# Kernel optimization log

Measured on AMD Instinct MI355X. Metric: run time of the kernel, lower is better.

The kernel has to match this reference:

```python
import jax, jax.numpy as jnp
import numpy as np

SAME_RANGE = 0.2  # depth tolerance for averaging splats at the same target pixel


def setup_inputs() -> dict:
    key = jax.random.key(0)
    k1, k2, k3 = jax.random.split(key, 3)
    B, C, H, W = 8, 3, 512, 1024
    obj = jax.random.normal(k1, (B, C, H, W), dtype=jnp.float32)
    flow = jax.random.normal(k2, (B, 2, H, W), dtype=jnp.float32)
    depth = jax.random.uniform(k3, (B, 1, H, W), dtype=jnp.float32)
    return {"obj": obj, "flow": flow, "depth": depth}


def reference(obj, flow, depth):
    # Forward-warping splat with per-target-pixel depth (z-buffer) test.
    # For each source pixel: warp by flow, round to nearest target pixel,
    # keep/average contributions whose depth is within same_range of the
    # minimum depth landing on that target pixel.
    B, C, H, W = obj.shape
    # p0: meshgrid with indexing='xy' stacked as (x, y) channels
    gx = jnp.arange(W, dtype=jnp.float32)[None, :]  # [1, W]
    gy = jnp.arange(H, dtype=jnp.float32)[:, None]  # [H, 1]
    p1x = gx + flow[:, 0]  # [B, H, W]
    p1y = gy + flow[:, 1]
    safe_x = jnp.clip(p1x, 0.0, W - 1)
    safe_y = jnp.clip(p1y, 0.0, H - 1)
    xi = jnp.round(safe_x).astype(jnp.int32)
    yi = jnp.round(safe_y).astype(jnp.int32)
    # flat target index, batch-offset so one segment op covers all batches
    boff = (jnp.arange(B, dtype=jnp.int32) * (H * W))[:, None, None]
    idx = (boff + yi * W + xi).reshape(-1)          # [B*H*W]
    d = depth.reshape(-1)                           # [B*H*W] (depth has 1 channel)
    n_seg = B * H * W
    # z-buffer: per-target minimum depth among all splatted source pixels
    dlut = jax.ops.segment_min(d, idx, num_segments=n_seg)
    # contributions within same_range of the winner are averaged
    keep = (d <= dlut[idx] + SAME_RANGE).astype(obj.dtype)  # [B*H*W]
    vals = obj.transpose(0, 2, 3, 1).reshape(-1, C)         # [B*H*W, C]
    sums = jax.ops.segment_sum(vals * keep[:, None], idx, num_segments=n_seg)
    cnts = jax.ops.segment_sum(keep, idx, num_segments=n_seg)
    out = jnp.where(cnts[:, None] > 0, sums / jnp.maximum(cnts[:, None], 1.0), 0.0)
    return out.reshape(B, H, W, C).transpose(0, 3, 1, 2)
```

## Files before the change

kernel.cpp:

```cpp
#include <hip/hip_runtime.h>

#define BB 8
#define CC 3
#define HH 512
#define WW 1024
#define HW (HH * WW)
#define NTOT (BB * HW)
#define SAME_RANGE 0.2f

#define R 4
#define TX 32
#define TY 32
#define TT (TX * TY)
#define RX (TX + 2 * R)
#define RY (TY + 2 * R)
#define QX (RX / 4)
#define NSLOT (RY * QX)
#define SLOT_ITERS 2
#define CAP 16384
#define D_SENTINEL 0x7F7F7F7F

#define FP_BIAS  16.0f
#define FP_SCALE 524288.0f

__device__ __forceinline__ unsigned int fp_enc(float v) {
    return (unsigned int)__float2uint_rn((v + FP_BIAS) * FP_SCALE);
}

__global__ __launch_bounds__(256) void gather_kernel(
        const float* __restrict__ obj,
        const float* __restrict__ flow,
        const float* __restrict__ depth,
        int* __restrict__ counter,
        float* __restrict__ list,
        float* __restrict__ out) {
    __shared__ int s_dmin[TT];
    __shared__ unsigned long long s_p01[TT];
    __shared__ unsigned long long s_p2c[TT];

    int lin = blockIdx.x + 32 * blockIdx.y + 512 * blockIdx.z;
    int wgid = (lin & 7) * 512 + (lin >> 3);
    int b   = wgid >> 9;
    int rr  = wgid & 511;
    int tx0 = (rr & 31) * TX;
    int ty0 = (rr >> 5) * TY;
    int tid = threadIdx.x;

    for (int i = tid; i < TT; i += 256) {
        s_dmin[i] = D_SENTINEL;
        s_p01[i] = 0ull;
        s_p2c[i] = 0ull;
    }
    __syncthreads();

    int   c_rem[SLOT_ITERS];
    int   c_tl[SLOT_ITERS][4];
    float c_d[SLOT_ITERS][4];

    #pragma unroll
    for (int it = 0; it < SLOT_ITERS; ++it) {
        int s = tid + it * 256;
        int remv = -1;
        int tl[4] = {-1, -1, -1, -1};
        float dv[4] = {0.0f, 0.0f, 0.0f, 0.0f};
        if (s < NSLOT) {
            int sy = s / QX;
            int sx4 = s - sy * QX;
            int gy = ty0 - R + sy;
            int gxb = tx0 - R + (sx4 << 2);
            if (gy >= 0 && gy < HH && gxb >= 0 && gxb < WW) {
                int rem = gy * WW + gxb;
                const float4 fx4 = *reinterpret_cast<const float4*>(flow + (size_t)(b * 2 + 0) * HW + rem);
                const float4 fy4 = *reinterpret_cast<const float4*>(flow + (size_t)(b * 2 + 1) * HW + rem);
                const float4 dd4 = *reinterpret_cast<const float4*>(depth + (size_t)b * HW + rem);
                float fxa[4] = {fx4.x, fx4.y, fx4.z, fx4.w};
                float fya[4] = {fy4.x, fy4.y, fy4.z, fy4.w};
                float dda[4] = {dd4.x, dd4.y, dd4.z, dd4.w};
                float gyf = (float)gy;
                remv = rem;
                #pragma unroll
                for (int j = 0; j < 4; ++j) {
                    int px = gxb + j;
                    float fx = fxa[j] + (float)px;
                    float fy = fya[j] + gyf;
                    fx = fminf(fmaxf(fx, 0.0f), (float)(WW - 1));
                    fy = fminf(fmaxf(fy, 0.0f), (float)(HH - 1));
                    int xi = (int)rintf(fx);
                    int yi = (int)rintf(fy);
                    int ddx = xi - px; if (ddx < 0) ddx = -ddx;
                    int ddy = yi - gy; if (ddy < 0) ddy = -ddy;
                    if (ddx <= R && ddy <= R) {
                        int lx = xi - tx0;
                        int ly = yi - ty0;
                        if (lx >= 0 && lx < TX && ly >= 0 && ly < TY) {
                            int tloc = ly * TX + lx;
                            tl[j] = tloc;
                            dv[j] = dda[j];
                            atomicMin(&s_dmin[tloc], __float_as_int(dda[j]));
                        }
                    } else if (px >= tx0 && px < tx0 + TX &&
                               gy >= ty0 && gy < ty0 + TY) {
                        int srem = rem + j;
                        int pos = atomicAdd(counter, 1);
                        if (pos < CAP) {
                            float* e = list + (size_t)pos * 8;
                            e[0] = __int_as_float(b * HW + yi * WW + xi);
                            e[1] = dda[j];
                            e[2] = obj[(b * CC + 0) * HW + srem];
                            e[3] = obj[(b * CC + 1) * HW + srem];
                            e[4] = obj[(b * CC + 2) * HW + srem];
                        }
                    }
                }
            }
        }
        c_rem[it] = remv;
        #pragma unroll
        for (int j = 0; j < 4; ++j) { c_tl[it][j] = tl[j]; c_d[it][j] = dv[j]; }
    }
    __syncthreads();

    #pragma unroll
    for (int it = 0; it < SLOT_ITERS; ++it) {
        int rem = c_rem[it];
        if (rem >= 0) {
            const float4 o04 = *reinterpret_cast<const float4*>(obj + (size_t)(b * CC + 0) * HW + rem);
            const float4 o14 = *reinterpret_cast<const float4*>(obj + (size_t)(b * CC + 1) * HW + rem);
            const float4 o24 = *reinterpret_cast<const float4*>(obj + (size_t)(b * CC + 2) * HW + rem);
            float o0a[4] = {o04.x, o04.y, o04.z, o04.w};
            float o1a[4] = {o14.x, o14.y, o14.z, o14.w};
            float o2a[4] = {o24.x, o24.y, o24.z, o24.w};
            #pragma unroll
            for (int j = 0; j < 4; ++j) {
                int t = c_tl[it][j];
                if (t >= 0) {
                    float thresh = __int_as_float(s_dmin[t]) + SAME_RANGE;
                    if (c_d[it][j] <= thresh) {
                        unsigned long long p01 =
                            (unsigned long long)fp_enc(o0a[j]) |
                            ((unsigned long long)fp_enc(o1a[j]) << 32);
                        unsigned long long p2c =
                            (unsigned long long)fp_enc(o2a[j]) | (1ull << 32);
                        atomicAdd(&s_p01[t], p01);
                        atomicAdd(&s_p2c[t], p2c);
                    }
                }
            }
        }
    }
    __syncthreads();

    for (int i = tid; i < TT; i += 256) {
        int lx = i & (TX - 1);
        int ly = i >> 5;
        int orem = (ty0 + ly) * WW + (tx0 + lx);
        unsigned long long p01 = s_p01[i];
        unsigned long long p2c = s_p2c[i];
        unsigned int cnt = (unsigned int)(p2c >> 32);
        float r0 = 0.0f, r1 = 0.0f, r2 = 0.0f;
        if (cnt > 0) {
            double inv = 1.0 / ((double)FP_SCALE * (double)cnt);
            r0 = (float)((double)(unsigned int)(p01 & 0xffffffffu) * inv - (double)FP_BIAS);
            r1 = (float)((double)(unsigned int)(p01 >> 32)         * inv - (double)FP_BIAS);
            r2 = (float)((double)(unsigned int)(p2c & 0xffffffffu) * inv - (double)FP_BIAS);
        }
        out[(b * CC + 0) * HW + orem] = r0;
        out[(b * CC + 1) * HW + orem] = r1;
        out[(b * CC + 2) * HW + orem] = r2;
    }
}

__global__ __launch_bounds__(64) void fixup_kernel(
        const float* __restrict__ obj,
        const float* __restrict__ flow,
        const float* __restrict__ depth,
        const int* __restrict__ counter,
        const float* __restrict__ list,
        float* __restrict__ out) {
    int noutl = *counter;
    if (noutl > CAP) noutl = CAP;
    int lane = threadIdx.x;
    for (int o = blockIdx.x; o < noutl; o += gridDim.x) {
        int tidx = __float_as_int(list[(size_t)o * 8]);
        int tb   = tidx >> 19;
        int trem = tidx & (HW - 1);
        int tyy  = trem >> 10;
        int txx  = trem & (WW - 1);
        float cd[2] = {0.0f, 0.0f};
        int   cr[2] = {-1, -1};
        float dmin = 1e30f;
        #pragma unroll
        for (int c = 0; c < 2; ++c) {
            int k = lane + c * 64;
            if (k < 81) {
                int ky = k / 9;
                int sy = tyy - R + ky;
                int sx = txx - R + (k - ky * 9);
                if (sx >= 0 && sx < WW && sy >= 0 && sy < HH) {
                    int srem = sy * WW + sx;
                    float fx = flow[(tb * 2 + 0) * HW + srem] + (float)sx;
                    float fy = flow[(tb * 2 + 1) * HW + srem] + (float)sy;
                    fx = fminf(fmaxf(fx, 0.0f), (float)(WW - 1));
                    fy = fminf(fmaxf(fy, 0.0f), (float)(HH - 1));
                    if ((int)rintf(fx) == txx && (int)rintf(fy) == tyy) {
                        float d = depth[tb * HW + srem];
                        cd[c] = d; cr[c] = srem;
                        dmin = fminf(dmin, d);
                    }
                }
            }
        }
        for (int k = lane; k < noutl; k += 64) {
            const float* e = list + (size_t)k * 8;
            if (__float_as_int(e[0]) == tidx) dmin = fminf(dmin, e[1]);
        }
        #pragma unroll
        for (int m = 32; m >= 1; m >>= 1)
            dmin = fminf(dmin, __shfl_xor(dmin, m));
        float thr = dmin + SAME_RANGE;
        float s0 = 0.0f, s1 = 0.0f, s2 = 0.0f, cnt = 0.0f;
        #pragma unroll
        for (int c = 0; c < 2; ++c) {
            if (cr[c] >= 0 && cd[c] <= thr) {
                s0 += obj[(tb * CC + 0) * HW + cr[c]];
                s1 += obj[(tb * CC + 1) * HW + cr[c]];
                s2 += obj[(tb * CC + 2) * HW + cr[c]];
                cnt += 1.0f;
            }
        }
        for (int k = lane; k < noutl; k += 64) {
            const float* e = list + (size_t)k * 8;
            if (__float_as_int(e[0]) == tidx && e[1] <= thr) {
                s0 += e[2]; s1 += e[3]; s2 += e[4]; cnt += 1.0f;
            }
        }
        #pragma unroll
        for (int m = 32; m >= 1; m >>= 1) {
            s0  += __shfl_xor(s0, m);
            s1  += __shfl_xor(s1, m);
            s2  += __shfl_xor(s2, m);
            cnt += __shfl_xor(cnt, m);
        }
        if (lane == 0) {
            out[(tb * CC + 0) * HW + trem] = s0 / cnt;
            out[(tb * CC + 1) * HW + trem] = s1 / cnt;
            out[(tb * CC + 2) * HW + trem] = s2 / cnt;
        }
    }
}

extern "C" void kernel_launch(void* const* d_in, const int* in_sizes, int n_in,
                              void* d_out, int out_size, void* d_ws, size_t ws_size,
                              hipStream_t stream) {
    const float* obj   = (const float*)d_in[0];
    const float* flow  = (const float*)d_in[1];
    const float* depth = (const float*)d_in[2];
    float* out = (float*)d_out;

    int*   counter = (int*)d_ws;
    float* list    = (float*)((char*)d_ws + 256);

    hipMemsetAsync(counter, 0, sizeof(int), stream);

    gather_kernel<<<dim3(WW / TX, HH / TY, BB), dim3(256), 0, stream>>>(
        obj, flow, depth, counter, list, out);

    fixup_kernel<<<dim3(64), dim3(64), 0, stream>>>(
        obj, flow, depth, counter, list, out);
}
```

Before: 153.1 us.

## Widen tiles to 64x32 with 512 threads, preload obj early, vectorize output

Result: no change. 150.7 us (-1.6%).

```diff
diff --git a/kernel.cpp b/kernel.cpp
--- a/kernel.cpp
+++ b/kernel.cpp
@@ -5,17 +5,17 @@
 #define HH 512
 #define WW 1024
 #define HW (HH * WW)
-#define NTOT (BB * HW)
 #define SAME_RANGE 0.2f
 
 #define R 4
-#define TX 32
+#define TX 64
 #define TY 32
 #define TT (TX * TY)
 #define RX (TX + 2 * R)
 #define RY (TY + 2 * R)
 #define QX (RX / 4)
 #define NSLOT (RY * QX)
+#define NTHREADS 512
 #define SLOT_ITERS 2
 #define CAP 16384
 #define D_SENTINEL 0x7F7F7F7F
@@ -27,7 +27,11 @@
     return (unsigned int)__float2uint_rn((v + FP_BIAS) * FP_SCALE);
 }
 
-__global__ __launch_bounds__(256) void gather_kernel(
+__device__ __forceinline__ float f4_get(const float4& v, int j) {
+    return j == 0 ? v.x : (j == 1 ? v.y : (j == 2 ? v.z : v.w));
+}
+
+__global__ __launch_bounds__(NTHREADS) void gather_kernel(
         const float* __restrict__ obj,
         const float* __restrict__ flow,
         const float* __restrict__ depth,
@@ -38,31 +42,35 @@
     __shared__ unsigned long long s_p01[TT];
     __shared__ unsigned long long s_p2c[TT];
 
-    int lin = blockIdx.x + 32 * blockIdx.y + 512 * blockIdx.z;
-    int wgid = (lin & 7) * 512 + (lin >> 3);
-    int b   = wgid >> 9;
-    int rr  = wgid & 511;
-    int tx0 = (rr & 31) * TX;
-    int ty0 = (rr >> 5) * TY;
+    int lin = blockIdx.x + 16 * blockIdx.y + 256 * blockIdx.z;
+    int wgid = (lin & 7) * 256 + (lin >> 3);
+    int b   = wgid >> 8;
+    int rr  = wgid & 255;
+    int tx0 = (rr & 15) * TX;
+    int ty0 = (rr >> 4) * TY;
     int tid = threadIdx.x;
 
-    for (int i = tid; i < TT; i += 256) {
+    for (int i = tid; i < TT; i += NTHREADS) {
         s_dmin[i] = D_SENTINEL;
         s_p01[i] = 0ull;
         s_p2c[i] = 0ull;
     }
     __syncthreads();
 
-    int   c_rem[SLOT_ITERS];
-    int   c_tl[SLOT_ITERS][4];
-    float c_d[SLOT_ITERS][4];
+    int    c_rem[SLOT_ITERS];
+    int    c_tl[SLOT_ITERS][4];
+    float  c_d[SLOT_ITERS][4];
+    float4 c_o0[SLOT_ITERS], c_o1[SLOT_ITERS], c_o2[SLOT_ITERS];
 
     #pragma unroll
     for (int it = 0; it < SLOT_ITERS; ++it) {
-        int s = tid + it * 256;
+        int s = tid + it * NTHREADS;
         int remv = -1;
         int tl[4] = {-1, -1, -1, -1};
         float dv[4] = {0.0f, 0.0f, 0.0f, 0.0f};
+        c_o0[it] = make_float4(0.f, 0.f, 0.f, 0.f);
+        c_o1[it] = make_float4(0.f, 0.f, 0.f, 0.f);
+        c_o2[it] = make_float4(0.f, 0.f, 0.f, 0.f);
         if (s < NSLOT) {
             int sy = s / QX;
             int sx4 = s - sy * QX;
@@ -73,42 +81,42 @@
                 const float4 fx4 = *reinterpret_cast<const float4*>(flow + (size_t)(b * 2 + 0) * HW + rem);
                 const float4 fy4 = *reinterpret_cast<const float4*>(flow + (size_t)(b * 2 + 1) * HW + rem);
                 const float4 dd4 = *reinterpret_cast<const float4*>(depth + (size_t)b * HW + rem);
-                float fxa[4] = {fx4.x, fx4.y, fx4.z, fx4.w};
-                float fya[4] = {fy4.x, fy4.y, fy4.z, fy4.w};
-                float dda[4] = {dd4.x, dd4.y, dd4.z, dd4.w};
+                c_o0[it] = *reinterpret_cast<const float4*>(obj + (size_t)(b * CC + 0) * HW + rem);
+                c_o1[it] = *reinterpret_cast<const float4*>(obj + (size_t)(b * CC + 1) * HW + rem);
+                c_o2[it] = *reinterpret_cast<const float4*>(obj + (size_t)(b * CC + 2) * HW + rem);
                 float gyf = (float)gy;
                 remv = rem;
                 #pragma unroll
                 for (int j = 0; j < 4; ++j) {
                     int px = gxb + j;
-                    float fx = fxa[j] + (float)px;
-                    float fy = fya[j] + gyf;
+                    float fx = f4_get(fx4, j) + (float)px;
+                    float fy = f4_get(fy4, j) + gyf;
                     fx = fminf(fmaxf(fx, 0.0f), (float)(WW - 1));
                     fy = fminf(fmaxf(fy, 0.0f), (float)(HH - 1));
                     int xi = (int)rintf(fx);
                     int yi = (int)rintf(fy);
                     int ddx = xi - px; if (ddx < 0) ddx = -ddx;
                     int ddy = yi - gy; if (ddy < 0) ddy = -ddy;
+                    float dj = f4_get(dd4, j);
                     if (ddx <= R && ddy <= R) {
                         int lx = xi - tx0;
                         int ly = yi - ty0;
                         if (lx >= 0 && lx < TX && ly >= 0 && ly < TY) {
                             int tloc = ly * TX + lx;
                             tl[j] = tloc;
-                            dv[j] = dda[j];
-                            atomicMin(&s_dmin[tloc], __float_as_int(dda[j]));
+                            dv[j] = dj;
+                            atomicMin(&s_dmin[tloc], __float_as_int(dj));
                         }
                     } else if (px >= tx0 && px < tx0 + TX &&
                                gy >= ty0 && gy < ty0 + TY) {
-                        int srem = rem + j;
                         int pos = atomicAdd(counter, 1);
                         if (pos < CAP) {
                             float* e = list + (size_t)pos * 8;
                             e[0] = __int_as_float(b * HW + yi * WW + xi);
-                            e[1] = dda[j];
-                            e[2] = obj[(b * CC + 0) * HW + srem];
-                            e[3] = obj[(b * CC + 1) * HW + srem];
-                            e[4] = obj[(b * CC + 2) * HW + srem];
+                            e[1] = dj;
+                            e[2] = f4_get(c_o0[it], j);
+                            e[3] = f4_get(c_o1[it], j);
+                            e[4] = f4_get(c_o2[it], j);
                         }
                     }
                 }
@@ -122,14 +130,7 @@
 
     #pragma unroll
     for (int it = 0; it < SLOT_ITERS; ++it) {
-        int rem = c_rem[it];
-        if (rem >= 0) {
-            const float4 o04 = *reinterpret_cast<const float4*>(obj + (size_t)(b * CC + 0) * HW + rem);
-            const float4 o14 = *reinterpret_cast<const float4*>(obj + (size_t)(b * CC + 1) * HW + rem);
-            const float4 o24 = *reinterpret_cast<const float4*>(obj + (size_t)(b * CC + 2) * HW + rem);
-            float o0a[4] = {o04.x, o04.y, o04.z, o04.w};
-            float o1a[4] = {o14.x, o14.y, o14.z, o14.w};
-            float o2a[4] = {o24.x, o24.y, o24.z, o24.w};
+        if (c_rem[it] >= 0) {
             #pragma unroll
             for (int j = 0; j < 4; ++j) {
                 int t = c_tl[it][j];
@@ -137,10 +138,10 @@
                     float thresh = __int_as_float(s_dmin[t]) + SAME_RANGE;
                     if (c_d[it][j] <= thresh) {
                         unsigned long long p01 =
-                            (unsigned long long)fp_enc(o0a[j]) |
-                            ((unsigned long long)fp_enc(o1a[j]) << 32);
+                            (unsigned long long)fp_enc(f4_get(c_o0[it], j)) |
+                            ((unsigned long long)fp_enc(f4_get(c_o1[it], j)) << 32);
                         unsigned long long p2c =
-                            (unsigned long long)fp_enc(o2a[j]) | (1ull << 32);
+                            (unsigned long long)fp_enc(f4_get(c_o2[it], j)) | (1ull << 32);
                         atomicAdd(&s_p01[t], p01);
                         atomicAdd(&s_p2c[t], p2c);
                     }
@@ -150,23 +151,31 @@
     }
     __syncthreads();
 
-    for (int i = tid; i < TT; i += 256) {
-        int lx = i & (TX - 1);
-        int ly = i >> 5;
-        int orem = (ty0 + ly) * WW + (tx0 + lx);
-        unsigned long long p01 = s_p01[i];
-        unsigned long long p2c = s_p2c[i];
-        unsigned int cnt = (unsigned int)(p2c >> 32);
-        float r0 = 0.0f, r1 = 0.0f, r2 = 0.0f;
-        if (cnt > 0) {
-            double inv = 1.0 / ((double)FP_SCALE * (double)cnt);
-            r0 = (float)((double)(unsigned int)(p01 & 0xffffffffu) * inv - (double)FP_BIAS);
-            r1 = (float)((double)(unsigned int)(p01 >> 32)         * inv - (double)FP_BIAS);
-            r2 = (float)((double)(unsigned int)(p2c & 0xffffffffu) * inv - (double)FP_BIAS);
-        }
-        out[(b * CC + 0) * HW + orem] = r0;
-        out[(b * CC + 1) * HW + orem] = r1;
-        out[(b * CC + 2) * HW + orem] = r2;
+    {
+        int base = tid << 2;
+        int lx = base & (TX - 1);
+        int ly = base >> 6;
+        int orow = (ty0 + ly) * WW + tx0 + lx;
+        float4 r0, r1, r2;
+        #pragma unroll
+        for (int k = 0; k < 4; ++k) {
+            unsigned long long p01 = s_p01[base + k];
+            unsigned long long p2c = s_p2c[base + k];
+            unsigned int cnt = (unsigned int)(p2c >> 32);
+            float f0 = 0.0f, f1 = 0.0f, f2 = 0.0f;
+            if (cnt > 0) {
+                float inv = (1.0f / FP_SCALE) / (float)cnt;
+                f0 = (float)(unsigned int)(p01 & 0xffffffffu) * inv - FP_BIAS;
+                f1 = (float)(unsigned int)(p01 >> 32)         * inv - FP_BIAS;
+                f2 = (float)(unsigned int)(p2c & 0xffffffffu) * inv - FP_BIAS;
+            }
+            ((float*)&r0)[k] = f0;
+            ((float*)&r1)[k] = f1;
+            ((float*)&r2)[k] = f2;
+        }
+        *reinterpret_cast<float4*>(out + (size_t)(b * CC + 0) * HW + orow) = r0;
+        *reinterpret_cast<float4*>(out + (size_t)(b * CC + 1) * HW + orow) = r1;
+        *reinterpret_cast<float4*>(out + (size_t)(b * CC + 2) * HW + orow) = r2;
     }
 }
 
@@ -262,7 +271,7 @@
 
     hipMemsetAsync(counter, 0, sizeof(int), stream);
 
-    gather_kernel<<<dim3(WW / TX, HH / TY, BB), dim3(256), 0, stream>>>(
+    gather_kernel<<<dim3(WW / TX, HH / TY, BB), dim3(NTHREADS), 0, stream>>>(
         obj, flow, depth, counter, list, out);
 
     fixup_kernel<<<dim3(64), dim3(64), 0, stream>>>(
```
